# Kernel tuning notes

Measured on AMD Instinct MI355X. Metric: run time of the kernel, lower is better.

## Reference

```python
import jax, jax.numpy as jnp
import numpy as np

DIM = 2048
HEADS = 16
HDIM = DIM // HEADS  # 128
B = 1
F, HG, WG = 5, 20, 32
L = F * HG * WG  # 3200
EPS = 1e-6
MAXPOS = 1024
C = HDIM // 2  # 64 rotary pairs
S0 = C - 2 * (C // 3)  # 22 (frame band)
S1 = C // 3            # 21 (height band)


def _rope_tables():
    # Matches Wan rope_params: per-band inverse-freq tables, angle = pos * inv_freq.
    pos = np.arange(MAXPOS, dtype=np.float64)
    chunks = []
    for s in (S0, S1, S1):
        d = 2 * s
        inv = 1.0 / (10000.0 ** (np.arange(0, d, 2, dtype=np.float64) / d))
        chunks.append(np.outer(pos, inv))
    ang = np.concatenate(chunks, axis=1)  # [MAXPOS, C]
    return np.cos(ang).astype(np.float32), np.sin(ang).astype(np.float32)


def setup_inputs() -> dict:
    key = jax.random.key(0)
    ks = jax.random.split(key, 6)
    sc = 1.0 / np.sqrt(DIM)
    fc, fs = _rope_tables()
    return {
        'x': jax.random.normal(ks[0], (B, L, DIM), dtype=jnp.float32),
        'wq': jax.random.normal(ks[1], (DIM, DIM), dtype=jnp.float32) * sc,
        'bq': jnp.zeros((DIM,), jnp.float32),
        'wk': jax.random.normal(ks[2], (DIM, DIM), dtype=jnp.float32) * sc,
        'bk': jnp.zeros((DIM,), jnp.float32),
        'wv': jax.random.normal(ks[3], (DIM, DIM), dtype=jnp.float32) * sc,
        'bv': jnp.zeros((DIM,), jnp.float32),
        'wo': jax.random.normal(ks[4], (DIM, DIM), dtype=jnp.float32) * sc,
        'bo': jnp.zeros((DIM,), jnp.float32),
        'norm_q_w': jnp.ones((DIM,), jnp.float32),
        'norm_k_w': jnp.ones((DIM,), jnp.float32),
        'freqs_cos': jnp.asarray(fc),
        'freqs_sin': jnp.asarray(fs),
    }


def _grid_freqs(tab):
    # Split bands and broadcast over the (F, HG, WG) grid -> [L, C]
    bf, bh, bw = tab[:, :S0], tab[:, S0:S0 + S1], tab[:, S0 + S1:]
    gf = jnp.broadcast_to(bf[:F, None, None, :], (F, HG, WG, S0))
    gh = jnp.broadcast_to(bh[None, :HG, None, :], (F, HG, WG, S1))
    gw = jnp.broadcast_to(bw[None, None, :WG, :], (F, HG, WG, S1))
    return jnp.concatenate([gf, gh, gw], axis=-1).reshape(L, C)


def reference(x, wq, bq, wk, bk, wv, bv, wo, bo, norm_q_w, norm_k_w, freqs_cos, freqs_sin):
    def rms(t, w):
        return t * jax.lax.rsqrt(jnp.mean(t * t, axis=-1, keepdims=True) + EPS) * w

    q = rms(x @ wq.T + bq, norm_q_w).reshape(B, L, HEADS, HDIM)
    k = rms(x @ wk.T + bk, norm_k_w).reshape(B, L, HEADS, HDIM)
    v = (x @ wv.T + bv).reshape(B, L, HEADS, HDIM)

    fc = _grid_freqs(freqs_cos)  # [L, C]
    fs = _grid_freqs(freqs_sin)

    def rope(t):
        tr = t.reshape(B, L, HEADS, C, 2)
        xr, xi = tr[..., 0], tr[..., 1]
        c = fc[None, :, None, :]
        s = fs[None, :, None, :]
        return jnp.stack([xr * c - xi * s, xr * s + xi * c], axis=-1).reshape(B, L, HEADS, HDIM)

    q = rope(q)
    k = rope(k)

    scores = jnp.einsum('blhd,bmhd->bhlm', q, k) / jnp.sqrt(jnp.float32(HDIM))
    attn = jax.nn.softmax(scores, axis=-1)
    out = jnp.einsum('bhlm,bmhd->blhd', attn, v).reshape(B, L, DIM)
    return out @ wo.T + bo
```

## Files before the change

### kernel.cpp

```cpp
#include <hip/hip_runtime.h>

typedef unsigned short u16;
typedef unsigned int u32;
typedef __attribute__((ext_vector_type(4))) float f32x4;
typedef __attribute__((ext_vector_type(8))) short bf16x8;
typedef __attribute__((ext_vector_type(8))) u16 u16x8;
typedef __attribute__((ext_vector_type(4))) u16 u16x4;
typedef __attribute__((ext_vector_type(4))) u32 u32x4;

#define GLOB_AS __attribute__((address_space(1)))
#define LDS_AS  __attribute__((address_space(3)))

__device__ __forceinline__ void gload_lds16(const void* g, void* l) {
  __builtin_amdgcn_global_load_lds((const GLOB_AS void*)g, (LDS_AS void*)l, 16, 0, 0);
}

__device__ __forceinline__ u16 f2bf(float f) {
  u32 u = __builtin_bit_cast(u32, f);
  u += 0x7fffu + ((u >> 16) & 1u);
  return (u16)(u >> 16);
}

__device__ __forceinline__ float bf2f(u16 b) {
  u32 u = (u32)b << 16;
  return __builtin_bit_cast(float, u);
}

#define MFMA16(a, b, c) __builtin_amdgcn_mfma_f32_16x16x32_bf16(a, b, c, 0, 0, 0)

__global__ __launch_bounds__(256) void cast_all(const float* __restrict__ x,
                                                const float* __restrict__ wq,
                                                const float* __restrict__ wk,
                                                const float* __restrict__ wv,
                                                const float* __restrict__ wo,
                                                u16* __restrict__ xb, u16* __restrict__ wqb,
                                                u16* __restrict__ wkb, u16* __restrict__ wvb,
                                                u16* __restrict__ wob) {
  int i = blockIdx.x * 256 + threadIdx.x;
  const float* s;
  u16* d;
  int off;
  if (i < 819200)       { s = x;  d = xb;  off = i; }
  else if (i < 1343488) { s = wq; d = wqb; off = i - 819200; }
  else if (i < 1867776) { s = wk; d = wkb; off = i - 1343488; }
  else if (i < 2392064) { s = wv; d = wvb; off = i - 1867776; }
  else                  { s = wo; d = wob; off = i - 2392064; }
  f32x4 a = ((const f32x4*)s)[2 * off], b = ((const f32x4*)s)[2 * off + 1];
  u16x8 o;
  o[0] = f2bf(a[0]); o[1] = f2bf(a[1]); o[2] = f2bf(a[2]); o[3] = f2bf(a[3]);
  o[4] = f2bf(b[0]); o[5] = f2bf(b[1]); o[6] = f2bf(b[2]); o[7] = f2bf(b[3]);
  ((u16x8*)d)[off] = o;
}

__global__ __launch_bounds__(256) void gemm_qkv(const u16* __restrict__ A,
                                                const u16* __restrict__ Bq,
                                                const u16* __restrict__ Bk,
                                                const u16* __restrict__ Bv,
                                                const float* __restrict__ bq,
                                                const float* __restrict__ bk,
                                                const float* __restrict__ bv,
                                                u16* __restrict__ Cq,
                                                u16* __restrict__ Ck,
                                                u16* __restrict__ Cv) {
  constexpr int K = 2048, N = 2048;
  __shared__ u16 As[128 * 64];
  __shared__ u16 Bs[128 * 64];
  const int tid = threadIdx.x;
  const int wave = tid >> 6, lane = tid & 63;
  const int lg = lane >> 4, li = lane & 15;
  const int lid = blockIdx.x + 25 * blockIdx.y;
  const int tile = (lid & 7) * 150 + (lid >> 3);
  const int bx = tile % 25, by = tile / 25;
  const int m0 = bx * 128;
  const int mat = by >> 4;
  const int n0 = (by & 15) * 128;
  const u16* B = (mat == 0) ? Bq : (mat == 1) ? Bk : Bv;
  const float* bias = (mat == 0) ? bq : (mat == 1) ? bk : bv;
  u16* C = (mat == 0) ? Cq : (mat == 1) ? Ck : Cv;
  const int wr = (wave >> 1) * 64, wc = (wave & 1) * 64;

  const u16* Ag = A + (size_t)(m0 + 32 * wave + (lane >> 3)) * K + (lane & 7) * 8;
  const u16* Bg = B + (size_t)(n0 + 32 * wave + (lane >> 3)) * K + (lane & 7) * 8;
  u16* AsW = As + wave * 2048;
  u16* BsW = Bs + wave * 2048;

  f32x4 acc[4][4] = {};
  for (int k0 = 0; k0 < K; k0 += 64) {
    __syncthreads();
#pragma unroll
    for (int j = 0; j < 4; ++j) {
      gload_lds16(Ag + k0 + (size_t)(8 * j) * K, AsW + j * 512);
      gload_lds16(Bg + k0 + (size_t)(8 * j) * K, BsW + j * 512);
    }
    __syncthreads();
#pragma unroll
    for (int kk = 0; kk < 64; kk += 32) {
      bf16x8 af[4], bfr[4];
#pragma unroll
      for (int mi = 0; mi < 4; mi++)
        af[mi] = *(const bf16x8*)&As[(wr + mi * 16 + li) * 64 + kk + lg * 8];
#pragma unroll
      for (int ni = 0; ni < 4; ni++)
        bfr[ni] = *(const bf16x8*)&Bs[(wc + ni * 16 + li) * 64 + kk + lg * 8];
#pragma unroll
      for (int mi = 0; mi < 4; mi++)
#pragma unroll
        for (int ni = 0; ni < 4; ni++)
          acc[mi][ni] = MFMA16(af[mi], bfr[ni], acc[mi][ni]);
    }
  }
  float bcol[4];
#pragma unroll
  for (int ni = 0; ni < 4; ni++) bcol[ni] = bias[n0 + wc + ni * 16 + li];
#pragma unroll
  for (int mi = 0; mi < 4; mi++) {
#pragma unroll
    for (int ni = 0; ni < 4; ni++) {
      const int gm = m0 + wr + mi * 16 + lg * 4;
      const int gn = n0 + wc + ni * 16 + li;
#pragma unroll
      for (int r = 0; r < 4; r++)
        C[(size_t)(gm + r) * N + gn] = f2bf(acc[mi][ni][r] + bcol[ni]);
    }
  }
}

__global__ __launch_bounds__(256) void gemm_nt(const u16* __restrict__ A,
                                               const u16* __restrict__ B,
                                               const float* __restrict__ bias,
                                               float* __restrict__ C) {
  constexpr int K = 2048, N = 2048;
  __shared__ u16 As[128 * 64];
  __shared__ u16 Bs[128 * 64];
  const int tid = threadIdx.x;
  const int wave = tid >> 6, lane = tid & 63;
  const int lg = lane >> 4, li = lane & 15;
  const int lid = blockIdx.x + 25 * blockIdx.y;
  const int tile = (lid & 7) * 50 + (lid >> 3);
  const int m0 = (tile % 25) * 128, n0 = (tile / 25) * 128;
  const int wr = (wave >> 1) * 64, wc = (wave & 1) * 64;

  const u16* Ag = A + (size_t)(m0 + 32 * wave + (lane >> 3)) * K + (lane & 7) * 8;
  const u16* Bg = B + (size_t)(n0 + 32 * wave + (lane >> 3)) * K + (lane & 7) * 8;
  u16* AsW = As + wave * 2048;
  u16* BsW = Bs + wave * 2048;

  f32x4 acc[4][4] = {};
  for (int k0 = 0; k0 < K; k0 += 64) {
    __syncthreads();
#pragma unroll
    for (int j = 0; j < 4; ++j) {
      gload_lds16(Ag + k0 + (size_t)(8 * j) * K, AsW + j * 512);
      gload_lds16(Bg + k0 + (size_t)(8 * j) * K, BsW + j * 512);
    }
    __syncthreads();
#pragma unroll
    for (int kk = 0; kk < 64; kk += 32) {
      bf16x8 af[4], bfr[4];
#pragma unroll
      for (int mi = 0; mi < 4; mi++)
        af[mi] = *(const bf16x8*)&As[(wr + mi * 16 + li) * 64 + kk + lg * 8];
#pragma unroll
      for (int ni = 0; ni < 4; ni++)
        bfr[ni] = *(const bf16x8*)&Bs[(wc + ni * 16 + li) * 64 + kk + lg * 8];
#pragma unroll
      for (int mi = 0; mi < 4; mi++)
#pragma unroll
        for (int ni = 0; ni < 4; ni++)
          acc[mi][ni] = MFMA16(af[mi], bfr[ni], acc[mi][ni]);
    }
  }
  float bcol[4];
#pragma unroll
  for (int ni = 0; ni < 4; ni++) bcol[ni] = bias[n0 + wc + ni * 16 + li];
#pragma unroll
  for (int mi = 0; mi < 4; mi++) {
#pragma unroll
    for (int ni = 0; ni < 4; ni++) {
      const int gm = m0 + wr + mi * 16 + lg * 4;
      const int gn = n0 + wc + ni * 16 + li;
#pragma unroll
      for (int r = 0; r < 4; r++)
        C[(size_t)(gm + r) * N + gn] = acc[mi][ni][r] + bcol[ni];
    }
  }
}

__global__ __launch_bounds__(256) void rms_rope2(const u16* __restrict__ preq,
                                                 const u16* __restrict__ prek,
                                                 const float* __restrict__ wq,
                                                 const float* __restrict__ wk,
                                                 const float* __restrict__ fcos,
                                                 const float* __restrict__ fsin,
                                                 u16* __restrict__ outq,
                                                 u16* __restrict__ outk, float foldq) {
  const int isk = blockIdx.x >= 3200;
  const int l = isk ? blockIdx.x - 3200 : blockIdx.x;
  const u16* pre = isk ? prek : preq;
  const float* w = isk ? wk : wq;
  u16* out = isk ? outk : outq;
  const float fold = isk ? 1.0f : foldq;
  const int tid = threadIdx.x;
  const int d0 = tid * 8;
  u16x8 pv = *(const u16x8*)(pre + (size_t)l * 2048 + d0);
  float xv[8];
#pragma unroll
  for (int j = 0; j < 8; j++) xv[j] = bf2f(pv[j]);
  float ss = (xv[0] * xv[0] + xv[1] * xv[1]) + (xv[2] * xv[2] + xv[3] * xv[3]) +
             (xv[4] * xv[4] + xv[5] * xv[5]) + (xv[6] * xv[6] + xv[7] * xv[7]);
#pragma unroll
  for (int m = 32; m; m >>= 1) ss += __shfl_xor(ss, m);
  __shared__ float red[4];
  if ((tid & 63) == 0) red[tid >> 6] = ss;
  __syncthreads();
  const float scale =
      rsqrtf((red[0] + red[1] + red[2] + red[3]) * (1.0f / 2048.0f) + 1e-6f) * fold;
  f32x4 w0 = *(const f32x4*)(w + d0);
  f32x4 w1 = *(const f32x4*)(w + d0 + 4);
  float xs[8];
#pragma unroll
  for (int j = 0; j < 4; j++) {
    xs[j] = xv[j] * w0[j] * scale;
    xs[4 + j] = xv[4 + j] * w1[j] * scale;
  }
  const int f = l / 640, rem = l % 640;
  const int hh = rem >> 5, ww = rem & 31;
  const int cb = (d0 & 127) >> 1;
  u16x8 ov;
#pragma unroll
  for (int i = 0; i < 4; i++) {
    const int c = cb + i;
    const int prow = c < 22 ? f : (c < 43 ? hh : ww);
    const float fc = fcos[prow * 64 + c];
    const float fs = fsin[prow * 64 + c];
    const float xr = xs[2 * i], xi = xs[2 * i + 1];
    ov[2 * i] = f2bf(xr * fc - xi * fs);
    ov[2 * i + 1] = f2bf(xr * fs + xi * fc);
  }
  *(u16x8*)(out + (size_t)l * 2048 + d0) = ov;
}

__global__ __launch_bounds__(256) void transpose_2d(const u16* __restrict__ src,
                                                    u16* __restrict__ dst) {
  __shared__ u16 t[64][72];
  const int m0 = blockIdx.x * 64, n0 = blockIdx.y * 64;
  const int tid = threadIdx.x;
  const int r = tid >> 3, c8 = (tid & 7) * 8;
#pragma unroll
  for (int j = 0; j < 2; j++) {
    u16x8 v = *(const u16x8*)&src[(size_t)(m0 + r + 32 * j) * 2048 + n0 + c8];
#pragma unroll
    for (int e = 0; e < 8; e++) t[c8 + e][r + 32 * j] = v[e];
  }
  __syncthreads();
  const int b = (c8 >> 5) * 32;
  const int cc = ((c8 >> 3) & 3) * 4;
#pragma unroll
  for (int j = 0; j < 2; j++) {
    const u16* trow = &t[r + 32 * j][0];
    u16x4 lo = *(const u16x4*)&trow[b + cc];
    u16x4 hi = *(const u16x4*)&trow[b + 16 + cc];
    u16x8 v;
    v[0] = lo[0]; v[1] = lo[1]; v[2] = lo[2]; v[3] = lo[3];
    v[4] = hi[0]; v[5] = hi[1]; v[6] = hi[2]; v[7] = hi[3];
    *(u16x8*)&dst[(size_t)(n0 + r + 32 * j) * 3200 + m0 + c8] = v;
  }
}

__global__ __launch_bounds__(256) void attn_kernel(const u16* __restrict__ Q,
                                                   const u16* __restrict__ Kb,
                                                   const u16* __restrict__ VT,
                                                   u16* __restrict__ O) {
  __shared__ u16 Klds[2][64 * 128];
  __shared__ u16 Vlds[2][128 * 64];
  const int tid = threadIdx.x, wave = tid >> 6, lane = tid & 63;
  const int lg = lane >> 4, li = lane & 15;

  const int lid = blockIdx.x + 50 * blockIdx.y;
  const int xcd = lid & 7, ixd = lid >> 3;
  const int h = xcd * 2 + (ixd & 1);
  const int qrow0 = (ixd >> 1) * 64 + wave * 16;

  bf16x8 qf[4];
  {
    const u16* qb = Q + (size_t)(qrow0 + li) * 2048 + h * 128 + lg * 8;
#pragma unroll
    for (int ks = 0; ks < 4; ks++) qf[ks] = *(const bf16x8*)(qb + ks * 32);
  }
  f32x4 o[8] = {};
  float mrow = -1e30f;
  float lrow = 0.f;

  const int klp = lane >> 4;
  const int kg0 = (lane & 15) ^ klp;
  const int kdg8 = ((kg0 ^ 4) - kg0) * 8;
  const u16* kp = Kb + (size_t)(wave * 16 + klp) * 2048 + h * 128 + kg0 * 8;
  const int vlp = lane >> 3;
  const int vg = (lane & 7) ^ vlp;
  const u16* vp = VT + (size_t)(h * 128 + wave * 32 + vlp) * 3200 + vg * 8;
  const u32 dstoff = wave * 2048 + lane * 8;
  int sb = 0;

#define STAGE()                                       \
  do {                                                \
    u16* kd = &Klds[sb][0] + dstoff;                  \
    u16* vd = &Vlds[sb][0] + dstoff;                  \
    gload_lds16(kp, kd);                              \
    gload_lds16(kp + 4 * 2048 + kdg8, kd + 512);      \
    gload_lds16(kp + 8 * 2048, kd + 1024);            \
    gload_lds16(kp + 12 * 2048 + kdg8, kd + 1536);    \
    gload_lds16(vp, vd);                              \
    gload_lds16(vp + 8 * 3200, vd + 512);             \
    gload_lds16(vp + 16 * 3200, vd + 1024);           \
    gload_lds16(vp + 24 * 3200, vd + 1536);           \
    kp += 64 * 2048;                                  \
    vp += 64;                                         \
    sb ^= 1;                                          \
  } while (0)

  STAGE();
  STAGE();

  for (int it = 0; it < 50; ++it) {
    const int buf = it & 1;
    if (it < 49)
      asm volatile("s_waitcnt vmcnt(8)" ::: "memory");
    else
      asm volatile("s_waitcnt vmcnt(0)" ::: "memory");
    __builtin_amdgcn_s_barrier();

    f32x4 s4[4] = {};
#pragma unroll
    for (int t = 0; t < 4; t++)
#pragma unroll
      for (int ks = 0; ks < 4; ks++) {
        const bf16x8 kf = *(const bf16x8*)&Klds[buf][(t * 16 + li) * 128 +
                                                     ((ks * 4 + lg) ^ (li & 7)) * 8];
        s4[t] = MFMA16(kf, qf[ks], s4[t]);
      }
    float pm = fmaxf(fmaxf(fmaxf(s4[0][0], s4[0][1]), fmaxf(s4[0][2], s4[0][3])),
                     fmaxf(fmaxf(s4[1][0], s4[1][1]), fmaxf(s4[1][2], s4[1][3])));
    pm = fmaxf(pm, fmaxf(fmaxf(fmaxf(s4[2][0], s4[2][1]), fmaxf(s4[2][2], s4[2][3])),
                         fmaxf(fmaxf(s4[3][0], s4[3][1]), fmaxf(s4[3][2], s4[3][3]))));
    pm = fmaxf(pm, __shfl_xor(pm, 16));
    pm = fmaxf(pm, __shfl_xor(pm, 32));
    if (__any(pm - mrow > 8.0f)) {
      const float mn = fmaxf(mrow, pm);
      const float alq = exp2f(mrow - mn);
      mrow = mn;
      lrow *= alq;
      float alv[4];
#pragma unroll
      for (int i = 0; i < 4; i++) alv[i] = __shfl(alq, lg * 4 + i);
#pragma unroll
      for (int f8 = 0; f8 < 8; f8++) {
        o[f8][0] *= alv[0]; o[f8][1] *= alv[1];
        o[f8][2] *= alv[2]; o[f8][3] *= alv[3];
      }
    }
    f32x4 p[4];
#pragma unroll
    for (int t = 0; t < 4; t++)
#pragma unroll
      for (int i = 0; i < 4; i++) p[t][i] = exp2f(s4[t][i] - mrow);
    lrow += ((p[0][0] + p[0][1]) + (p[0][2] + p[0][3])) +
            ((p[1][0] + p[1][1]) + (p[1][2] + p[1][3])) +
            ((p[2][0] + p[2][1]) + (p[2][2] + p[2][3])) +
            ((p[3][0] + p[3][1]) + (p[3][2] + p[3][3]));
    u32 wp[8];
    asm("v_cvt_pk_bf16_f32 %0, %1, %2" : "=v"(wp[0]) : "v"(p[0][0]), "v"(p[0][1]));
    asm("v_cvt_pk_bf16_f32 %0, %1, %2" : "=v"(wp[1]) : "v"(p[0][2]), "v"(p[0][3]));
    asm("v_cvt_pk_bf16_f32 %0, %1, %2" : "=v"(wp[2]) : "v"(p[1][0]), "v"(p[1][1]));
    asm("v_cvt_pk_bf16_f32 %0, %1, %2" : "=v"(wp[3]) : "v"(p[1][2]), "v"(p[1][3]));
    asm("v_cvt_pk_bf16_f32 %0, %1, %2" : "=v"(wp[4]) : "v"(p[2][0]), "v"(p[2][1]));
    asm("v_cvt_pk_bf16_f32 %0, %1, %2" : "=v"(wp[5]) : "v"(p[2][2]), "v"(p[2][3]));
    asm("v_cvt_pk_bf16_f32 %0, %1, %2" : "=v"(wp[6]) : "v"(p[3][0]), "v"(p[3][1]));
    asm("v_cvt_pk_bf16_f32 %0, %1, %2" : "=v"(wp[7]) : "v"(p[3][2]), "v"(p[3][3]));
    u32x4 paw0 = {wp[0], wp[1], wp[2], wp[3]};
    u32x4 paw1 = {wp[4], wp[5], wp[6], wp[7]};
    const bf16x8 pa0 = __builtin_bit_cast(bf16x8, paw0);
    const bf16x8 pa1 = __builtin_bit_cast(bf16x8, paw1);

#pragma unroll
    for (int tt = 0; tt < 2; tt++)
#pragma unroll
      for (int f8 = 0; f8 < 8; f8++) {
        const bf16x8 vf = *(const bf16x8*)&Vlds[buf][(f8 * 16 + li) * 64 +
                                                     ((tt * 4 + lg) ^ (li & 7)) * 8];
        o[f8] = MFMA16(tt ? pa1 : pa0, vf, o[f8]);
      }
    __builtin_amdgcn_s_barrier();
    if (it <= 47) STAGE();
  }
#undef STAGE

  float lt = lrow;
  lt += __shfl_xor(lt, 16);
  lt += __shfl_xor(lt, 32);
  const float inv = 1.0f / lt;
  float invi[4];
#pragma unroll
  for (int i = 0; i < 4; i++) invi[i] = __shfl(inv, lg * 4 + i);
#pragma unroll
  for (int i = 0; i < 4; i++) {
    const int row = qrow0 + lg * 4 + i;
#pragma unroll
    for (int f8 = 0; f8 < 8; f8++)
      O[(size_t)row * 2048 + h * 128 + f8 * 16 + li] = f2bf(o[f8][i] * invi[i]);
  }
}

extern "C" void kernel_launch(void* const* d_in, const int* in_sizes, int n_in,
                              void* d_out, int out_size, void* d_ws, size_t ws_size,
                              hipStream_t stream) {
  const float* x    = (const float*)d_in[0];
  const float* wq   = (const float*)d_in[1];
  const float* bq   = (const float*)d_in[2];
  const float* wk   = (const float*)d_in[3];
  const float* bk   = (const float*)d_in[4];
  const float* wv   = (const float*)d_in[5];
  const float* bv   = (const float*)d_in[6];
  const float* wo   = (const float*)d_in[7];
  const float* bo   = (const float*)d_in[8];
  const float* nqw  = (const float*)d_in[9];
  const float* nkw  = (const float*)d_in[10];
  const float* fcos = (const float*)d_in[11];
  const float* fsin = (const float*)d_in[12];

  const size_t NEED = 125304832;
  if (ws_size < NEED) return;
  char* ws = (char*)d_ws;
  u16* x_bf   = (u16*)(ws + 0);
  u16* wq_bf  = (u16*)(ws + 13107200);
  u16* wk_bf  = (u16*)(ws + 21495808);
  u16* wv_bf  = (u16*)(ws + 29884416);
  u16* wo_bf  = (u16*)(ws + 38273024);
  u16* preq   = (u16*)(ws + 46661632);
  u16* prek   = (u16*)(ws + 59768832);
  u16* v_bf   = (u16*)(ws + 72876032);
  u16* q_bf   = (u16*)(ws + 85983232);
  u16* k_bf   = (u16*)(ws + 99090432);
  u16* vT     = (u16*)(ws + 112197632);
  u16* att_bf = (u16*)(ws + 46661632);

  cast_all<<<11392, 256, 0, stream>>>(x, wq, wk, wv, wo, x_bf, wq_bf, wk_bf, wv_bf,
                                      wo_bf);

  const float foldq = 1.4426950408889634f * 0.08838834764831843f;

  gemm_qkv<<<dim3(25, 48), 256, 0, stream>>>(x_bf, wq_bf, wk_bf, wv_bf, bq, bk, bv,
                                             preq, prek, v_bf);
  rms_rope2<<<6400, 256, 0, stream>>>(preq, prek, nqw, nkw, fcos, fsin, q_bf, k_bf,
                                      foldq);
  transpose_2d<<<dim3(50, 32), 256, 0, stream>>>(v_bf, vT);
  attn_kernel<<<dim3(50, 16), 256, 0, stream>>>(q_bf, k_bf, vT, att_bf);
  gemm_nt<<<dim3(25, 16), 256, 0, stream>>>(att_bf, wo_bf, bo, (float*)d_out);
}
```

Baseline: 383.6 us.

## Double-buffer LDS tiles in QKV and output GEMMs with async prefetch

```diff
diff --git a/kernel.cpp b/kernel.cpp
--- a/kernel.cpp
+++ b/kernel.cpp
@@ -52,6 +52,72 @@
   ((u16x8*)d)[off] = o;
 }
 
+#define GEMM_BODY(C_WRITE)                                                        \
+  f32x4 acc[4][4] = {};                                                           \
+  const u32 dstoff = wave * 2048 + lane * 8;       \
+  int gsb = 0;                                                                    \
+  const u16* Agp = Ag;                                                            \
+  const u16* Bgp = Bg;                                                            \
+  _Pragma("unroll") for (int pf = 0; pf < 2; ++pf) {                              \
+    u16* ad = &As[gsb][0] + dstoff;                                               \
+    u16* bd = &Bs[gsb][0] + dstoff;                                               \
+    gload_lds16(Agp, ad);                                                         \
+    gload_lds16(Agp + (size_t)8 * K, ad + 512);                                   \
+    gload_lds16(Agp + (size_t)16 * K, ad + 1024);                                 \
+    gload_lds16(Agp + (size_t)24 * K, ad + 1536);                                 \
+    gload_lds16(Bgp, bd);                                                         \
+    gload_lds16(Bgp + (size_t)8 * K, bd + 512);                                   \
+    gload_lds16(Bgp + (size_t)16 * K, bd + 1024);                                 \
+    gload_lds16(Bgp + (size_t)24 * K, bd + 1536);                                 \
+    Agp += 64;                                                                    \
+    Bgp += 64;                                                                    \
+    gsb ^= 1;                                                                     \
+  }                                                                               \
+  for (int it = 0; it < 32; ++it) {                                               \
+    const int buf = it & 1;                                                       \
+    if (it < 31)                                                                  \
+      asm volatile("s_waitcnt vmcnt(8)" ::: "memory");                            \
+    else                                                                          \
+      asm volatile("s_waitcnt vmcnt(0)" ::: "memory");                            \
+    __builtin_amdgcn_s_barrier();                                                 \
+    _Pragma("unroll") for (int kk = 0; kk < 64; kk += 32) {                       \
+      bf16x8 af[4], bfr[4];                                                       \
+      _Pragma("unroll") for (int mi = 0; mi < 4; mi++)                            \
+          af[mi] = *(const bf16x8*)&As[buf][(wr + mi * 16 + li) * 64 + kk + lg * 8]; \
+      _Pragma("unroll") for (int ni = 0; ni < 4; ni++)                            \
+          bfr[ni] = *(const bf16x8*)&Bs[buf][(wc + ni * 16 + li) * 64 + kk + lg * 8]; \
+      _Pragma("unroll") for (int mi = 0; mi < 4; mi++)                            \
+          _Pragma("unroll") for (int ni = 0; ni < 4; ni++)                        \
+              acc[mi][ni] = MFMA16(af[mi], bfr[ni], acc[mi][ni]);                 \
+    }                                                                             \
+    __builtin_amdgcn_s_barrier();                                                 \
+    if (it <= 29) {                                                               \
+      u16* ad = &As[gsb][0] + dstoff;                                             \
+      u16* bd = &Bs[gsb][0] + dstoff;                                             \
+      gload_lds16(Agp, ad);                                                       \
+      gload_lds16(Agp + (size_t)8 * K, ad + 512);                                 \
+      gload_lds16(Agp + (size_t)16 * K, ad + 1024);                               \
+      gload_lds16(Agp + (size_t)24 * K, ad + 1536);                               \
+      gload_lds16(Bgp, bd);                                                       \
+      gload_lds16(Bgp + (size_t)8 * K, bd + 512);                                 \
+      gload_lds16(Bgp + (size_t)16 * K, bd + 1024);                               \
+      gload_lds16(Bgp + (size_t)24 * K, bd + 1536);                               \
+      Agp += 64;                                                                  \
+      Bgp += 64;                                                                  \
+      gsb ^= 1;                                                                   \
+    }                                                                             \
+  }                                                                               \
+  float bcol[4];                                                                  \
+  _Pragma("unroll") for (int ni = 0; ni < 4; ni++)                                \
+      bcol[ni] = bias[n0 + wc + ni * 16 + li];                                    \
+  _Pragma("unroll") for (int mi = 0; mi < 4; mi++) {                              \
+    _Pragma("unroll") for (int ni = 0; ni < 4; ni++) {                            \
+      const int gm = m0 + wr + mi * 16 + lg * 4;                                  \
+      const int gn = n0 + wc + ni * 16 + li;                                      \
+      _Pragma("unroll") for (int r = 0; r < 4; r++) { C_WRITE; }                  \
+    }                                                                             \
+  }
+
 __global__ __launch_bounds__(256) void gemm_qkv(const u16* __restrict__ A,
                                                 const u16* __restrict__ Bq,
                                                 const u16* __restrict__ Bk,
@@ -63,8 +129,8 @@
                                                 u16* __restrict__ Ck,
                                                 u16* __restrict__ Cv) {
   constexpr int K = 2048, N = 2048;
-  __shared__ u16 As[128 * 64];
-  __shared__ u16 Bs[128 * 64];
+  __shared__ u16 As[2][128 * 64];
+  __shared__ u16 Bs[2][128 * 64];
   const int tid = threadIdx.x;
   const int wave = tid >> 6, lane = tid & 63;
   const int lg = lane >> 4, li = lane & 15;
@@ -81,48 +147,8 @@
 
   const u16* Ag = A + (size_t)(m0 + 32 * wave + (lane >> 3)) * K + (lane & 7) * 8;
   const u16* Bg = B + (size_t)(n0 + 32 * wave + (lane >> 3)) * K + (lane & 7) * 8;
-  u16* AsW = As + wave * 2048;
-  u16* BsW = Bs + wave * 2048;
-
-  f32x4 acc[4][4] = {};
-  for (int k0 = 0; k0 < K; k0 += 64) {
-    __syncthreads();
-#pragma unroll
-    for (int j = 0; j < 4; ++j) {
-      gload_lds16(Ag + k0 + (size_t)(8 * j) * K, AsW + j * 512);
-      gload_lds16(Bg + k0 + (size_t)(8 * j) * K, BsW + j * 512);
-    }
-    __syncthreads();
-#pragma unroll
-    for (int kk = 0; kk < 64; kk += 32) {
-      bf16x8 af[4], bfr[4];
-#pragma unroll
-      for (int mi = 0; mi < 4; mi++)
-        af[mi] = *(const bf16x8*)&As[(wr + mi * 16 + li) * 64 + kk + lg * 8];
-#pragma unroll
-      for (int ni = 0; ni < 4; ni++)
-        bfr[ni] = *(const bf16x8*)&Bs[(wc + ni * 16 + li) * 64 + kk + lg * 8];
-#pragma unroll
-      for (int mi = 0; mi < 4; mi++)
-#pragma unroll
-        for (int ni = 0; ni < 4; ni++)
-          acc[mi][ni] = MFMA16(af[mi], bfr[ni], acc[mi][ni]);
-    }
-  }
-  float bcol[4];
-#pragma unroll
-  for (int ni = 0; ni < 4; ni++) bcol[ni] = bias[n0 + wc + ni * 16 + li];
-#pragma unroll
-  for (int mi = 0; mi < 4; mi++) {
-#pragma unroll
-    for (int ni = 0; ni < 4; ni++) {
-      const int gm = m0 + wr + mi * 16 + lg * 4;
-      const int gn = n0 + wc + ni * 16 + li;
-#pragma unroll
-      for (int r = 0; r < 4; r++)
-        C[(size_t)(gm + r) * N + gn] = f2bf(acc[mi][ni][r] + bcol[ni]);
-    }
-  }
+
+  GEMM_BODY(C[(size_t)(gm + r) * N + gn] = f2bf(acc[mi][ni][r] + bcol[ni]))
 }
 
 __global__ __launch_bounds__(256) void gemm_nt(const u16* __restrict__ A,
@@ -130,8 +156,8 @@
                                                const float* __restrict__ bias,
                                                float* __restrict__ C) {
   constexpr int K = 2048, N = 2048;
-  __shared__ u16 As[128 * 64];
-  __shared__ u16 Bs[128 * 64];
+  __shared__ u16 As[2][128 * 64];
+  __shared__ u16 Bs[2][128 * 64];
   const int tid = threadIdx.x;
   const int wave = tid >> 6, lane = tid & 63;
   const int lg = lane >> 4, li = lane & 15;
@@ -142,48 +168,8 @@
 
   const u16* Ag = A + (size_t)(m0 + 32 * wave + (lane >> 3)) * K + (lane & 7) * 8;
   const u16* Bg = B + (size_t)(n0 + 32 * wave + (lane >> 3)) * K + (lane & 7) * 8;
-  u16* AsW = As + wave * 2048;
-  u16* BsW = Bs + wave * 2048;
-
-  f32x4 acc[4][4] = {};
-  for (int k0 = 0; k0 < K; k0 += 64) {
-    __syncthreads();
-#pragma unroll
-    for (int j = 0; j < 4; ++j) {
-      gload_lds16(Ag + k0 + (size_t)(8 * j) * K, AsW + j * 512);
-      gload_lds16(Bg + k0 + (size_t)(8 * j) * K, BsW + j * 512);
-    }
-    __syncthreads();
-#pragma unroll
-    for (int kk = 0; kk < 64; kk += 32) {
-      bf16x8 af[4], bfr[4];
-#pragma unroll
-      for (int mi = 0; mi < 4; mi++)
-        af[mi] = *(const bf16x8*)&As[(wr + mi * 16 + li) * 64 + kk + lg * 8];
-#pragma unroll
-      for (int ni = 0; ni < 4; ni++)
-        bfr[ni] = *(const bf16x8*)&Bs[(wc + ni * 16 + li) * 64 + kk + lg * 8];
-#pragma unroll
-      for (int mi = 0; mi < 4; mi++)
-#pragma unroll
-        for (int ni = 0; ni < 4; ni++)
-          acc[mi][ni] = MFMA16(af[mi], bfr[ni], acc[mi][ni]);
-    }
-  }
-  float bcol[4];
-#pragma unroll
-  for (int ni = 0; ni < 4; ni++) bcol[ni] = bias[n0 + wc + ni * 16 + li];
-#pragma unroll
-  for (int mi = 0; mi < 4; mi++) {
-#pragma unroll
-    for (int ni = 0; ni < 4; ni++) {
-      const int gm = m0 + wr + mi * 16 + lg * 4;
-      const int gn = n0 + wc + ni * 16 + li;
-#pragma unroll
-      for (int r = 0; r < 4; r++)
-        C[(size_t)(gm + r) * N + gn] = acc[mi][ni][r] + bcol[ni];
-    }
-  }
+
+  GEMM_BODY(C[(size_t)(gm + r) * N + gn] = acc[mi][ni][r] + bcol[ni])
 }
 
 __global__ __launch_bounds__(256) void rms_rope2(const u16* __restrict__ preq,
```

New measurement: 376.7 us. About the same (-1.8%).
